# Kernel tuning notes

Hardware: AMD Instinct MI355X
Metric: run time of the kernel (lower is better)

The kernel has to match this reference:

```python
import jax, jax.numpy as jnp
import numpy as np

NUM_GRIDS = 16
IN_X, IN_Z, OUT, BATCH = 32, 32, 64, 512


def _borders_cdf_grid(n_chunks):
    def inv_cdf(u):
        return np.log(2.0 * u) if u <= 0.5 else -np.log(2.0 * (1.0 - u))
    cs = 1.0 / n_chunks
    b = [inv_cdf(i * cs) for i in range(1, n_chunks)]
    left = b[0] - (b[1] - b[0])
    right = b[-1] + (b[-1] - b[-2])
    return np.array([left] + b + [right], dtype=np.float32)


def _laplace_cdf(v):
    e = jnp.exp(-jnp.abs(v))
    return jnp.where(v > 0, 1.0 - 0.5 * e, 0.5 * e)


def setup_inputs() -> dict:
    key = jax.random.key(0)
    k1, k2, k3 = jax.random.split(key, 3)
    scale = 0.1 / np.sqrt(IN_X * IN_Z)
    borders_np = _borders_cdf_grid(NUM_GRIDS)
    inv_len_np = (1.0 / (borders_np[1:] - borders_np[:-1])).astype(np.float32)
    return {
        "x": jax.random.normal(k1, (IN_X, BATCH), dtype=jnp.float32),
        "z": jax.random.normal(k2, (IN_Z, BATCH), dtype=jnp.float32),
        "func_parameter": jax.random.uniform(
            k3, (NUM_GRIDS + 1, NUM_GRIDS + 1, OUT, IN_X, IN_Z),
            dtype=jnp.float32, minval=-scale, maxval=scale),
        "borders": jnp.asarray(borders_np),
        "inverse_chunk_lengths": jnp.asarray(inv_len_np[:NUM_GRIDS]),
    }


def reference(x, z, func_parameter, borders, inverse_chunk_lengths):
    G = inverse_chunk_lengths.shape[0]
    Ix, B = x.shape
    Iz = z.shape[0]

    # data-dependent bin indices per (input_dim, batch) element
    idx_x = jnp.clip((_laplace_cdf(x) * G).astype(jnp.int32), 0, G - 1)  # [Ix,B]
    idx_z = jnp.clip((_laplace_cdf(z) * G).astype(jnp.int32), 0, G - 1)  # [Iz,B]
    dx = (x - borders[idx_x]) * inverse_chunk_lengths[idx_x]             # [Ix,B]
    dz = (z - borders[idx_z]) * inverse_chunk_lengths[idx_z]             # [Iz,B]
    idx_xn = jnp.clip(idx_x + 1, 0, G)
    idx_zn = jnp.clip(idx_z + 1, 0, G)

    # [Ix, Iz, G+1, G+1, O] so the per-(ix,iz) tables are leading-indexed
    Pt = jnp.transpose(func_parameter, (3, 4, 0, 1, 2))
    ax = jnp.arange(Ix)[:, None, None]   # [Ix,1,1]
    az = jnp.arange(Iz)[None, :, None]   # [1,Iz,1]

    def corner(ii, jj):  # ii:[Ix,1,B] or broadcastable, jj:[1,Iz,B]
        return Pt[ax, az, ii, jj]        # -> [Ix,Iz,B,O]

    ixb, ixnb = idx_x[:, None, :], idx_xn[:, None, :]
    izb, iznb = idx_z[None, :, :], idx_zn[None, :, :]
    wx, wz = dx[:, None, :], dz[None, :, :]             # [Ix,1,B],[1,Iz,B]

    out = (
        jnp.einsum('xzb,xzbo->ob', (1 - wx) * (1 - wz), corner(ixb, izb))
        + jnp.einsum('xzb,xzbo->ob', (1 - wx) * wz, corner(ixb, iznb))
        + jnp.einsum('xzb,xzbo->ob', wx * (1 - wz), corner(ixnb, izb))
        + jnp.einsum('xzb,xzbo->ob', wx * wz, corner(ixnb, iznb))
    )
    return out  # [output_dim, batch]
```

## Files before the change

### kernel.cpp

```cpp
#include <hip/hip_runtime.h>
#include <hip/hip_fp16.h>


#define NG        16
#define NB        17
#define IN_X      32
#define IN_Z      32
#define OUT_DIM   64
#define BATCH     512
#define CELLS     (NB * NB)
#define LDS_STR   33
#define XSTR      (NB * LDS_STR)

__device__ __forceinline__ void grid_coord(float v,
                                           const float* __restrict__ borders,
                                           const float* __restrict__ inv_len,
                                           int& idx, float& w) {
    float e   = expf(-fabsf(v));
    float cdf = (v > 0.f) ? (1.f - 0.5f * e) : (0.5f * e);
    int t = (int)(cdf * 16.f);
    t = t < 0 ? 0 : (t > NG - 1 ? NG - 1 : t);
    idx = t;
    w = (v - borders[t]) * inv_len[t];
}

__device__ __forceinline__ __half2 u2h(unsigned u) {
    union { unsigned u; __half2 h; } v; v.u = u; return v.h;
}
__device__ __forceinline__ unsigned h2u(__half2 h) {
    union { unsigned u; __half2 h; } v; v.h = h; return v.u;
}

__global__ void precompute_kernel(const float* __restrict__ x,
                                  const float* __restrict__ z,
                                  const float* __restrict__ borders,
                                  const float* __restrict__ inv_len,
                                  float2* __restrict__ xc,
                                  uint2* __restrict__ zc,
                                  float* __restrict__ out) {
    const int gid = blockIdx.x * blockDim.x + threadIdx.x;
    out[gid] = 0.f;
    int idx; float w;
    if (gid < IN_X * BATCH) {
        grid_coord(x[gid], borders, inv_len, idx, w);
        xc[gid] = make_float2(w, __int_as_float(idx * XSTR));
    } else {
        const int g = gid - IN_X * BATCH;
        grid_coord(z[g], borders, inv_len, idx, w);
        zc[g] = make_uint2(h2u(__float2half2_rn(w)),
                           (unsigned)(idx * LDS_STR));
    }
}

__global__ __launch_bounds__(512, 8)
void bf2d_kernel(const float2* __restrict__ xc,
                 const uint2* __restrict__ zc,
                 const float* __restrict__ P,
                 float* __restrict__ out) {
    __shared__ unsigned lds[CELLS * LDS_STR];

    const int tid = threadIdx.x;
    const int o0  = (blockIdx.x & 31) * 2;
    const int i   = blockIdx.x >> 5;

    const float* Pbase = P + ((size_t)o0 * (IN_X * IN_Z) + (size_t)i * IN_Z);
    for (int k = tid; k < CELLS * IN_Z; k += 512) {
        const int c = k >> 5;
        const int j = k & 31;
        const size_t g = (size_t)c * (OUT_DIM * IN_X * IN_Z) + j;
        lds[c * LDS_STR + j] =
            h2u(__floats2half2_rn(Pbase[g], Pbase[g + IN_X * IN_Z]));
    }
    __syncthreads();

    const float2  xcv = xc[i * BATCH + tid];
    const __half2 wx2 = __float2half2_rn(xcv.x);
    const int    xoff = __float_as_int(xcv.y);

    const uint2* zp = zc + tid;
    float accx = 0.f, accy = 0.f;
    #pragma unroll 8
    for (int j = 0; j < IN_Z; ++j) {
        const uint2   zcv = zp[j * BATCH];
        const __half2 wz2 = u2h(zcv.x);
        const int    base = xoff + (int)zcv.y + j;
        const __half2 a0 = u2h(lds[base]);
        const __half2 a1 = u2h(lds[base + LDS_STR]);
        const __half2 b0 = u2h(lds[base + XSTR]);
        const __half2 b1 = u2h(lds[base + XSTR + LDS_STR]);
        const __half2 lo = __hfma2(wz2, __hsub2(a1, a0), a0);
        const __half2 hi = __hfma2(wz2, __hsub2(b1, b0), b0);
        const __half2 r  = __hfma2(wx2, __hsub2(hi, lo), lo);
        const float2  f  = __half22float2(r);
        accx += f.x;
        accy += f.y;
    }

    atomicAdd(&out[o0 * BATCH + tid],       accx);
    atomicAdd(&out[(o0 + 1) * BATCH + tid], accy);
}

extern "C" void kernel_launch(void* const* d_in, const int* in_sizes, int n_in,
                              void* d_out, int out_size, void* d_ws, size_t ws_size,
                              hipStream_t stream) {
    const float* x       = (const float*)d_in[0];
    const float* z       = (const float*)d_in[1];
    const float* P       = (const float*)d_in[2];
    const float* borders = (const float*)d_in[3];
    const float* inv_len = (const float*)d_in[4];
    float* out = (float*)d_out;

    float2* xc = (float2*)d_ws;
    uint2*  zc = (uint2*)(xc + IN_X * BATCH);

    precompute_kernel<<<dim3(128), dim3(256), 0, stream>>>(
        x, z, borders, inv_len, xc, zc, out);

    bf2d_kernel<<<dim3((OUT_DIM / 2) * IN_X), dim3(512), 0, stream>>>(
        xc, zc, P, out);
}
```

Baseline: 128.1 us.

## Process two input-x slices per block with overlapped staging and vectorized loads

Each block now handles two consecutive input-x slices with two LDS tables. It prefetches the second slice's parameters into registers while gathering from the first, which overlaps global loads with LDS gather work. Parameter loads become float4 vectors, and the z coordinates are transposed to batch-major so each thread reads them as uint4. This halves the block count and the number of atomics, but doubles the LDS per block and raises register use, with occupancy lowered to 4 waves per SIMD.

```diff
diff --git a/kernel.cpp b/kernel.cpp
--- a/kernel.cpp
+++ b/kernel.cpp
@@ -11,6 +11,8 @@
 #define CELLS     (NB * NB)
 #define LDS_STR   33
 #define XSTR      (NB * LDS_STR)
+#define QT        (CELLS * 8)
+#define NITER     5
 
 __device__ __forceinline__ void grid_coord(float v,
                                            const float* __restrict__ borders,
@@ -36,7 +38,7 @@
                                   const float* __restrict__ borders,
                                   const float* __restrict__ inv_len,
                                   float2* __restrict__ xc,
-                                  uint2* __restrict__ zc,
+                                  uint2* __restrict__ zc2,
                                   float* __restrict__ out) {
     const int gid = blockIdx.x * blockDim.x + threadIdx.x;
     out[gid] = 0.f;
@@ -46,54 +48,129 @@
         xc[gid] = make_float2(w, __int_as_float(idx * XSTR));
     } else {
         const int g = gid - IN_X * BATCH;
+        const int j = g >> 9;
+        const int b = g & (BATCH - 1);
         grid_coord(z[g], borders, inv_len, idx, w);
-        zc[g] = make_uint2(h2u(__float2half2_rn(w)),
-                           (unsigned)(idx * LDS_STR));
+        zc2[b * IN_Z + j] = make_uint2(h2u(__float2half2_rn(w)),
+                                       (unsigned)(idx * LDS_STR));
     }
 }
 
-__global__ __launch_bounds__(512, 8)
+__device__ __forceinline__ void gather_slice(const unsigned* __restrict__ S,
+                                             const uint4* __restrict__ zp4,
+                                             const __half2 wx2, const int xoff,
+                                             float& ax, float& ay) {
+    #pragma unroll 4
+    for (int jj = 0; jj < 16; ++jj) {
+        const uint4 q = zp4[jj];
+        {
+            const int base = xoff + (int)q.y + 2 * jj;
+            const __half2 wz2 = u2h(q.x);
+            const __half2 a0 = u2h(S[base]);
+            const __half2 a1 = u2h(S[base + LDS_STR]);
+            const __half2 b0 = u2h(S[base + XSTR]);
+            const __half2 b1 = u2h(S[base + XSTR + LDS_STR]);
+            const __half2 lo = __hfma2(wz2, __hsub2(a1, a0), a0);
+            const __half2 hi = __hfma2(wz2, __hsub2(b1, b0), b0);
+            const __half2 r  = __hfma2(wx2, __hsub2(hi, lo), lo);
+            const float2 f = __half22float2(r);
+            ax += f.x; ay += f.y;
+        }
+        {
+            const int base = xoff + (int)q.w + 2 * jj + 1;
+            const __half2 wz2 = u2h(q.z);
+            const __half2 a0 = u2h(S[base]);
+            const __half2 a1 = u2h(S[base + LDS_STR]);
+            const __half2 b0 = u2h(S[base + XSTR]);
+            const __half2 b1 = u2h(S[base + XSTR + LDS_STR]);
+            const __half2 lo = __hfma2(wz2, __hsub2(a1, a0), a0);
+            const __half2 hi = __hfma2(wz2, __hsub2(b1, b0), b0);
+            const __half2 r  = __hfma2(wx2, __hsub2(hi, lo), lo);
+            const float2 f = __half22float2(r);
+            ax += f.x; ay += f.y;
+        }
+    }
+}
+
+__global__ __launch_bounds__(512, 4)
 void bf2d_kernel(const float2* __restrict__ xc,
-                 const uint2* __restrict__ zc,
+                 const uint2* __restrict__ zc2,
                  const float* __restrict__ P,
                  float* __restrict__ out) {
-    __shared__ unsigned lds[CELLS * LDS_STR];
+    __shared__ unsigned ldsA[CELLS * LDS_STR];
+    __shared__ unsigned ldsB[CELLS * LDS_STR];
 
     const int tid = threadIdx.x;
-    const int o0  = (blockIdx.x & 31) * 2;
-    const int i   = blockIdx.x >> 5;
+    const int o0  = (blockIdx.x >> 4) * 2;
+    const int i0  = (blockIdx.x & 15) * 2;
+    const int i1  = i0 + 1;
 
-    const float* Pbase = P + ((size_t)o0 * (IN_X * IN_Z) + (size_t)i * IN_Z);
-    for (int k = tid; k < CELLS * IN_Z; k += 512) {
-        const int c = k >> 5;
-        const int j = k & 31;
-        const size_t g = (size_t)c * (OUT_DIM * IN_X * IN_Z) + j;
-        lds[c * LDS_STR + j] =
-            h2u(__floats2half2_rn(Pbase[g], Pbase[g + IN_X * IN_Z]));
+    const float* Pb = P + (size_t)o0 * 1024;
+
+    float4 r0[NITER], r1[NITER];
+
+    #pragma unroll
+    for (int t = 0; t < NITER; ++t) {
+        const int k = tid + t * 512;
+        if (k < QT) {
+            const int c = k >> 3, j4 = (k & 7) << 2;
+            const float* g = Pb + (size_t)c * 65536 + i0 * 32 + j4;
+            r0[t] = *(const float4*)g;
+            r1[t] = *(const float4*)(g + 1024);
+        }
+    }
+    #pragma unroll
+    for (int t = 0; t < NITER; ++t) {
+        const int k = tid + t * 512;
+        if (k < QT) {
+            const int c = k >> 3, j4 = (k & 7) << 2;
+            unsigned* d = &ldsA[c * LDS_STR + j4];
+            d[0] = h2u(__floats2half2_rn(r0[t].x, r1[t].x));
+            d[1] = h2u(__floats2half2_rn(r0[t].y, r1[t].y));
+            d[2] = h2u(__floats2half2_rn(r0[t].z, r1[t].z));
+            d[3] = h2u(__floats2half2_rn(r0[t].w, r1[t].w));
+        }
     }
     __syncthreads();
 
-    const float2  xcv = xc[i * BATCH + tid];
-    const __half2 wx2 = __float2half2_rn(xcv.x);
-    const int    xoff = __float_as_int(xcv.y);
+    #pragma unroll
+    for (int t = 0; t < NITER; ++t) {
+        const int k = tid + t * 512;
+        if (k < QT) {
+            const int c = k >> 3, j4 = (k & 7) << 2;
+            const float* g = Pb + (size_t)c * 65536 + i1 * 32 + j4;
+            r0[t] = *(const float4*)g;
+            r1[t] = *(const float4*)(g + 1024);
+        }
+    }
 
-    const uint2* zp = zc + tid;
+    const uint4* zp4 = (const uint4*)(zc2 + (size_t)tid * IN_Z);
     float accx = 0.f, accy = 0.f;
-    #pragma unroll 8
-    for (int j = 0; j < IN_Z; ++j) {
-        const uint2   zcv = zp[j * BATCH];
-        const __half2 wz2 = u2h(zcv.x);
-        const int    base = xoff + (int)zcv.y + j;
-        const __half2 a0 = u2h(lds[base]);
-        const __half2 a1 = u2h(lds[base + LDS_STR]);
-        const __half2 b0 = u2h(lds[base + XSTR]);
-        const __half2 b1 = u2h(lds[base + XSTR + LDS_STR]);
-        const __half2 lo = __hfma2(wz2, __hsub2(a1, a0), a0);
-        const __half2 hi = __hfma2(wz2, __hsub2(b1, b0), b0);
-        const __half2 r  = __hfma2(wx2, __hsub2(hi, lo), lo);
-        const float2  f  = __half22float2(r);
-        accx += f.x;
-        accy += f.y;
+
+    {
+        const float2 xcv = xc[i0 * BATCH + tid];
+        gather_slice(ldsA, zp4, __float2half2_rn(xcv.x),
+                     __float_as_int(xcv.y), accx, accy);
+    }
+
+    #pragma unroll
+    for (int t = 0; t < NITER; ++t) {
+        const int k = tid + t * 512;
+        if (k < QT) {
+            const int c = k >> 3, j4 = (k & 7) << 2;
+            unsigned* d = &ldsB[c * LDS_STR + j4];
+            d[0] = h2u(__floats2half2_rn(r0[t].x, r1[t].x));
+            d[1] = h2u(__floats2half2_rn(r0[t].y, r1[t].y));
+            d[2] = h2u(__floats2half2_rn(r0[t].z, r1[t].z));
+            d[3] = h2u(__floats2half2_rn(r0[t].w, r1[t].w));
+        }
+    }
+    __syncthreads();
+
+    {
+        const float2 xcv = xc[i1 * BATCH + tid];
+        gather_slice(ldsB, zp4, __float2half2_rn(xcv.x),
+                     __float_as_int(xcv.y), accx, accy);
     }
 
     atomicAdd(&out[o0 * BATCH + tid],       accx);
@@ -110,12 +187,12 @@
     const float* inv_len = (const float*)d_in[4];
     float* out = (float*)d_out;
 
-    float2* xc = (float2*)d_ws;
-    uint2*  zc = (uint2*)(xc + IN_X * BATCH);
+    float2* xc  = (float2*)d_ws;
+    uint2*  zc2 = (uint2*)(xc + IN_X * BATCH);
 
     precompute_kernel<<<dim3(128), dim3(256), 0, stream>>>(
-        x, z, borders, inv_len, xc, zc, out);
+        x, z, borders, inv_len, xc, zc2, out);
 
-    bf2d_kernel<<<dim3((OUT_DIM / 2) * IN_X), dim3(512), 0, stream>>>(
-        xc, zc, P, out);
+    bf2d_kernel<<<dim3((OUT_DIM / 2) * (IN_X / 2)), dim3(512), 0, stream>>>(
+        xc, zc2, P, out);
 }
```

Result: no change. 129.1 us (+0.8%).
